# Performance work log

Hardware: AMD Instinct MI355X
Metric: run time of the kernel (lower is better)

## Reference

```python
import jax, jax.numpy as jnp
import numpy as np

N_NODES = 100000
N_EDGES = 1600000
IN_RAW = 64
HID = 128


def setup_inputs() -> dict:
    key = jax.random.key(0)
    ks = jax.random.split(key, 16)
    inp = {
        "x": jax.random.normal(ks[0], (N_NODES, IN_RAW), dtype=jnp.float32),
        "edge_index": jax.random.randint(ks[1], (2, N_EDGES), 0, N_NODES, dtype=jnp.int64),
        "user_ids": jax.random.randint(ks[2], (N_NODES,), 0, 10000, dtype=jnp.int64),
        "locations": jax.random.randint(ks[3], (N_NODES,), 0, 1000, dtype=jnp.int64),
        "time_features": jax.random.normal(ks[4], (N_NODES, 4), dtype=jnp.float32),
        # embeddings / encoders
        "user_emb_table": jax.random.normal(ks[5], (10000, 32), dtype=jnp.float32) * 0.02,
        "loc_emb_table": jax.random.normal(ks[6], (1000, 16), dtype=jnp.float32) * 0.02,
        "W_time": jax.random.normal(ks[7], (4, 16), dtype=jnp.float32) * 0.1,
        "b_time": jnp.zeros((16,), dtype=jnp.float32),
        # SAGEConv 1: lin_l (aggregated, with bias), lin_r (root, no bias)
        "W1_l": jax.random.normal(ks[8], (HID, HID), dtype=jnp.float32) * (1.0 / np.sqrt(HID)),
        "b1": jnp.zeros((HID,), dtype=jnp.float32),
        "W1_r": jax.random.normal(ks[9], (HID, HID), dtype=jnp.float32) * (1.0 / np.sqrt(HID)),
        # SAGEConv 2
        "W2_l": jax.random.normal(ks[10], (HID, HID), dtype=jnp.float32) * (1.0 / np.sqrt(HID)),
        "b2": jnp.zeros((HID,), dtype=jnp.float32),
        "W2_r": jax.random.normal(ks[11], (HID, HID), dtype=jnp.float32) * (1.0 / np.sqrt(HID)),
        # classifier
        "Wc": jax.random.normal(ks[12], (HID, 1), dtype=jnp.float32) * (1.0 / np.sqrt(HID)),
        "bc": jnp.zeros((1,), dtype=jnp.float32),
    }
    return inp


def _sage_conv(h, src, dst, W_l, b_l, W_r, n_nodes):
    # mean aggregation of source features onto targets (PyG SAGEConv default)
    msg_sum = jax.ops.segment_sum(h[src], dst, num_segments=n_nodes)  # [N, D]
    deg = jax.ops.segment_sum(jnp.ones((src.shape[0],), h.dtype), dst, num_segments=n_nodes)
    agg = msg_sum / jnp.maximum(deg, 1.0)[:, None]
    return agg @ W_l + b_l + h @ W_r


def reference(x, edge_index, user_ids, locations, time_features,
              user_emb_table, loc_emb_table, W_time, b_time,
              W1_l, b1, W1_r, W2_l, b2, W2_r, Wc, bc):
    n = x.shape[0]
    src, dst = edge_index[0], edge_index[1]
    user_emb = user_emb_table[user_ids]            # [N, 32]
    loc_emb = loc_emb_table[locations]             # [N, 16]
    time_emb = time_features @ W_time + b_time     # [N, 16]
    h = jnp.concatenate([x, user_emb, loc_emb, time_emb], axis=-1)  # [N, 128]
    h = jax.nn.relu(_sage_conv(h, src, dst, W1_l, b1, W1_r, n))  # dropout = identity (eval)
    h = jax.nn.relu(_sage_conv(h, src, dst, W2_l, b2, W2_r, n))
    return jax.nn.sigmoid(h @ Wc + bc)  # [N, 1]
```

## Files before the change

kernel.cpp:

```cpp
#include <hip/hip_runtime.h>
#include <math.h>

#define N_NODES 100000
#define HID 128
#define NB 782
#define CAP 4096
#define NBLK 196
#define BTILE 8192
#define SUBCAP 32
#define SCAP 3072
#define EMBB 3125
#define WPB 32

typedef __attribute__((ext_vector_type(8))) short bf16x8;
typedef __attribute__((ext_vector_type(4))) float f32x4;
typedef __attribute__((ext_vector_type(2))) float f32x2;

__device__ __forceinline__ unsigned short f2bf(float f) {
  union { float f; unsigned u; } v; v.f = f;
  unsigned r = v.u + 0x7FFFu + ((v.u >> 16) & 1u);
  return (unsigned short)(r >> 16);
}
__device__ __forceinline__ unsigned packbf(float lo, float hi) {
  return (unsigned)f2bf(lo) | ((unsigned)f2bf(hi) << 16);
}
__device__ __forceinline__ unsigned pkfp8x4(float a, float b, float c, float d) {
  int v = __builtin_amdgcn_cvt_pk_fp8_f32(a, b, 0, false);
  v = __builtin_amdgcn_cvt_pk_fp8_f32(c, d, v, true);
  return (unsigned)v;
}
__device__ __forceinline__ float bflo(unsigned u) {
  union { unsigned u; float f; } v; v.u = u << 16; return v.f;
}
__device__ __forceinline__ float bfhi(unsigned u) {
  union { unsigned u; float f; } v; v.u = u & 0xFFFF0000u; return v.f;
}
__device__ __forceinline__ void acc_add_fp8(float* a, unsigned w) {
  f32x2 p0 = __builtin_amdgcn_cvt_pk_f32_fp8((int)w, false);
  f32x2 p1 = __builtin_amdgcn_cvt_pk_f32_fp8((int)w, true);
  a[0] += p0.x; a[1] += p0.y; a[2] += p1.x; a[3] += p1.y;
}
__device__ __forceinline__ void acc_add_row(float* a, uint4 u) {
  acc_add_fp8(a + 0, u.x);
  acc_add_fp8(a + 4, u.y);
  acc_add_fp8(a + 8, u.z);
  acc_add_fp8(a + 12, u.w);
}

__global__ __launch_bounds__(512) void k_front(
    const float* __restrict__ x, const int* __restrict__ uid,
    const int* __restrict__ lid, const float* __restrict__ timef,
    const float* __restrict__ utab, const float* __restrict__ ltab,
    const float* __restrict__ Wt, const float* __restrict__ bt,
    unsigned short* __restrict__ h0, unsigned char* __restrict__ h0f8,
    const float* __restrict__ W1l, const float* __restrict__ W1r,
    const float* __restrict__ W2l, const float* __restrict__ W2r,
    unsigned short* __restrict__ WT,
    const int* __restrict__ src, const int* __restrict__ dst,
    int* __restrict__ gcnt, unsigned* __restrict__ bdata2, int E) {
  __shared__ int hcnt[NB];
  int bid = blockIdx.x;
  int t = threadIdx.x;

  if (bid < NBLK) {
    int e0 = bid * BTILE;
    int e1 = min(e0 + BTILE, E);
    for (int i = t; i < NB; i += 512) hcnt[i] = 0;
    __syncthreads();
#pragma unroll 4
    for (int e = e0 + t; e < e1; e += 512) atomicAdd(&hcnt[dst[e] >> 7], 1);
    __syncthreads();
    for (int i = t; i < NB; i += 512) {
      gcnt[bid * NB + i] = hcnt[i];
      hcnt[i] = 0;
    }
    __syncthreads();
#pragma unroll 4
    for (int e = e0 + t; e < e1; e += 512) {
      int d = dst[e], s = src[e];
      int b = d >> 7;
      int pos = atomicAdd(&hcnt[b], 1);
      if (pos < SUBCAP)
        bdata2[((size_t)bid * NB + b) * SUBCAP + pos] =
            ((unsigned)s << 7) | (unsigned)(d & 127);
    }
    return;
  }
  bid -= NBLK;

  if (bid < EMBB) {
    int v = bid * 32 + (t >> 4);
    int g = t & 15;
    if (v >= N_NODES) return;
    float val[8];
    if (g < 8) {
      const float4* xp = (const float4*)&x[(size_t)v * 64 + g * 8];
      float4 a = xp[0], b = xp[1];
      val[0] = a.x; val[1] = a.y; val[2] = a.z; val[3] = a.w;
      val[4] = b.x; val[5] = b.y; val[6] = b.z; val[7] = b.w;
    } else if (g < 12) {
      const float4* up = (const float4*)&utab[(size_t)uid[v] * 32 + (g - 8) * 8];
      float4 a = up[0], b = up[1];
      val[0] = a.x; val[1] = a.y; val[2] = a.z; val[3] = a.w;
      val[4] = b.x; val[5] = b.y; val[6] = b.z; val[7] = b.w;
    } else if (g < 14) {
      const float4* lp = (const float4*)&ltab[(size_t)lid[v] * 16 + (g - 12) * 8];
      float4 a = lp[0], b = lp[1];
      val[0] = a.x; val[1] = a.y; val[2] = a.z; val[3] = a.w;
      val[4] = b.x; val[5] = b.y; val[6] = b.z; val[7] = b.w;
    } else {
      int c0 = (g - 14) * 8;
      float4 tf = *(const float4*)&timef[(size_t)v * 4];
#pragma unroll
      for (int i = 0; i < 8; ++i) {
        int c = c0 + i;
        val[i] = bt[c] + tf.x * Wt[c] + tf.y * Wt[16 + c] + tf.z * Wt[32 + c] +
                 tf.w * Wt[48 + c];
      }
    }
    uint4 ob;
    ob.x = packbf(val[0], val[1]);
    ob.y = packbf(val[2], val[3]);
    ob.z = packbf(val[4], val[5]);
    ob.w = packbf(val[6], val[7]);
    *(uint4*)&h0[(size_t)v * 128 + g * 8] = ob;
    uint2 of;
    of.x = pkfp8x4(val[0], val[1], val[2], val[3]);
    of.y = pkfp8x4(val[4], val[5], val[6], val[7]);
    *(uint2*)&h0f8[(size_t)v * 128 + g * 8] = of;
    return;
  }
  bid -= EMBB;

  {
    int lin = (bid * 512 + t) * 4;
    int m = lin >> 14;
    int rem = lin & 16383;
    int f = rem >> 7;
    int k0 = rem & 127;
    const float* W = (m == 0) ? W1l : (m == 1) ? W1r : (m == 2) ? W2l : W2r;
    unsigned short o[4];
#pragma unroll
    for (int j = 0; j < 4; ++j) o[j] = f2bf(W[(size_t)(k0 + j) * 128 + f]);
    uint2 pk;
    pk.x = (unsigned)o[0] | ((unsigned)o[1] << 16);
    pk.y = (unsigned)o[2] | ((unsigned)o[3] << 16);
    *(uint2*)&WT[m * 16384 + f * 128 + k0] = pk;
  }
}

__global__ __launch_bounds__(256) void k_bfill(
    const int* __restrict__ gcnt, const unsigned* __restrict__ bdata2,
    int* __restrict__ rstart, int* __restrict__ rdeg, int* __restrict__ col) {
  __shared__ unsigned sdata[SCAP];
  __shared__ int soff[NBLK];
  __shared__ int scnt[NBLK];
  __shared__ int wsum[4];
  __shared__ int lcnt[128];
  __shared__ int wtot;
  int b = blockIdx.x;
  int t = threadIdx.x;
  int lane = t & 63, wv = t >> 6;

  int c = (t < NBLK) ? min(gcnt[t * NB + b], SUBCAP) : 0;
  int x = c;
#pragma unroll
  for (int off = 1; off < 64; off <<= 1) {
    int v = __shfl_up(x, off);
    if (lane >= off) x += v;
  }
  if (lane == 63) wsum[wv] = x;
  __syncthreads();
  int add = 0;
#pragma unroll
  for (int k = 0; k < 4; ++k)
    if (k < wv) add += wsum[k];
  x += add;
  int tot = min(wsum[0] + wsum[1] + wsum[2] + wsum[3], SCAP);
  if (t < NBLK) { soff[t] = x - c; scnt[t] = c; }
  if (t < 128) lcnt[t] = 0;
  __syncthreads();

  for (int i = t; i < NBLK * 8; i += 256) {
    int j = i >> 3, p4 = (i & 7) * 4;
    int cj = scnt[j];
    if (p4 < cj) {
      uint4 v = *(const uint4*)&bdata2[((size_t)j * NB + b) * SUBCAP + p4];
      int bs = soff[j] + p4;
      int n = min(4, cj - p4);
      unsigned vv[4] = {v.x, v.y, v.z, v.w};
#pragma unroll
      for (int e = 0; e < 4; ++e)
        if (e < n && bs + e < SCAP) sdata[bs + e] = vv[e];
    }
  }
  __syncthreads();

  for (int i = t; i < tot; i += 256) atomicAdd(&lcnt[sdata[i] & 127u], 1);
  __syncthreads();

  int node0 = b * 128;
  int base = b * CAP;
  if (t < 128) {
    int cc = lcnt[t];
    int xx = cc;
#pragma unroll
    for (int off = 1; off < 64; off <<= 1) {
      int v = __shfl_up(xx, off);
      if (lane >= off) xx += v;
    }
    if (t == 63) wtot = xx;
    __syncthreads();
    if (t >= 64) xx += wtot;
    int excl = xx - cc;
    if (node0 + t < N_NODES) {
      rstart[node0 + t] = base + excl;
      rdeg[node0 + t] = cc;
    }
    lcnt[t] = excl;
  } else {
    __syncthreads();
  }
  __syncthreads();
  for (int i = t; i < tot; i += 256) {
    unsigned v = sdata[i];
    int pos = base + atomicAdd(&lcnt[v & 127u], 1);
    col[pos] = (int)(v >> 7);
  }
}

__global__ __launch_bounds__(256) void k_agg(
    const unsigned char* __restrict__ hf8, const int* __restrict__ rstart,
    const int* __restrict__ rdeg, const int* __restrict__ col,
    unsigned short* __restrict__ agg) {
  int t = threadIdx.x;
  int v = blockIdx.x * 32 + (t >> 3);
  int q = t & 7;
  if (v >= N_NODES) return;
  int s0 = rstart[v];
  int deg = rdeg[v];
  int s1 = s0 + deg;
  const uint4* h8 = (const uint4*)hf8;
  float acc[16];
#pragma unroll
  for (int i = 0; i < 16; ++i) acc[i] = 0.f;
  int j = s0;
  for (; j + 8 <= s1; j += 8) {
    uint4 r0 = h8[(size_t)col[j] * 8 + q];
    uint4 r1 = h8[(size_t)col[j + 1] * 8 + q];
    uint4 r2 = h8[(size_t)col[j + 2] * 8 + q];
    uint4 r3 = h8[(size_t)col[j + 3] * 8 + q];
    uint4 r4 = h8[(size_t)col[j + 4] * 8 + q];
    uint4 r5 = h8[(size_t)col[j + 5] * 8 + q];
    uint4 r6 = h8[(size_t)col[j + 6] * 8 + q];
    uint4 r7 = h8[(size_t)col[j + 7] * 8 + q];
    acc_add_row(acc, r0);
    acc_add_row(acc, r1);
    acc_add_row(acc, r2);
    acc_add_row(acc, r3);
    acc_add_row(acc, r4);
    acc_add_row(acc, r5);
    acc_add_row(acc, r6);
    acc_add_row(acc, r7);
  }
  for (; j < s1; ++j) acc_add_row(acc, h8[(size_t)col[j] * 8 + q]);
  float inv = 1.f / (float)(deg > 0 ? deg : 1);
  uint4 o0, o1;
  o0.x = packbf(acc[0] * inv, acc[1] * inv);
  o0.y = packbf(acc[2] * inv, acc[3] * inv);
  o0.z = packbf(acc[4] * inv, acc[5] * inv);
  o0.w = packbf(acc[6] * inv, acc[7] * inv);
  o1.x = packbf(acc[8] * inv, acc[9] * inv);
  o1.y = packbf(acc[10] * inv, acc[11] * inv);
  o1.z = packbf(acc[12] * inv, acc[13] * inv);
  o1.w = packbf(acc[14] * inv, acc[15] * inv);
  ((uint4*)agg)[(size_t)v * 16 + q * 2] = o0;
  ((uint4*)agg)[(size_t)v * 16 + q * 2 + 1] = o1;
}

template <bool CLS>
__global__ __launch_bounds__(256, 4) void k_gemm(
    const unsigned short* __restrict__ agg, const unsigned short* __restrict__ hin,
    const unsigned short* __restrict__ WlT, const unsigned short* __restrict__ WrT,
    const float* __restrict__ bias, unsigned short* __restrict__ hout,
    unsigned char* __restrict__ houtf8,
    const float* __restrict__ Wc, const float* __restrict__ bc,
    float* __restrict__ out) {
  __shared__ unsigned short SB[2 * 64 * 136];
  unsigned short* As = SB;
  unsigned short* Hs = SB + 64 * 136;
  unsigned short* Ot = SB;
  float* zred = (float*)SB;
  int t = threadIdx.x;
  int lane = t & 63;
  int wave = t >> 6;
  int wn = wave * 32;
  int l15 = lane & 15;
  int quad = lane >> 4;
  int mbase = blockIdx.x * 64;

  {
    int r = t >> 2, seg = t & 3;
    int gn = mbase + r;
    uint4 av[4], hv[4];
    if (gn < N_NODES) {
      const uint4* ap = (const uint4*)(agg + (size_t)gn * 128 + seg * 32);
      const uint4* hp = (const uint4*)(hin + (size_t)gn * 128 + seg * 32);
#pragma unroll
      for (int i = 0; i < 4; ++i) { av[i] = ap[i]; hv[i] = hp[i]; }
    } else {
#pragma unroll
      for (int i = 0; i < 4; ++i) { av[i] = make_uint4(0,0,0,0); hv[i] = make_uint4(0,0,0,0); }
    }
#pragma unroll
    for (int i = 0; i < 4; ++i) {
      *(uint4*)&As[r * 136 + seg * 32 + i * 8] = av[i];
      *(uint4*)&Hs[r * 136 + seg * 32 + i * 8] = hv[i];
    }
  }
  __syncthreads();

  f32x4 acc4[4][2];
#pragma unroll
  for (int i = 0; i < 4; ++i)
#pragma unroll
    for (int j = 0; j < 2; ++j) acc4[i][j] = (f32x4){0.f, 0.f, 0.f, 0.f};

#pragma unroll
  for (int ks = 0; ks < 4; ++ks) {
    int kb = ks * 32 + quad * 8;
    bf16x8 bL[2], bR[2];
#pragma unroll
    for (int jn = 0; jn < 2; ++jn) {
      int f = wn + jn * 16 + l15;
      bL[jn] = *(const bf16x8*)&WlT[(size_t)f * 128 + kb];
      bR[jn] = *(const bf16x8*)&WrT[(size_t)f * 128 + kb];
    }
    bf16x8 aA[4], aH[4];
#pragma unroll
    for (int im = 0; im < 4; ++im) {
      aA[im] = *(const bf16x8*)&As[(im * 16 + l15) * 136 + kb];
      aH[im] = *(const bf16x8*)&Hs[(im * 16 + l15) * 136 + kb];
    }
#pragma unroll
    for (int im = 0; im < 4; ++im)
#pragma unroll
      for (int jn = 0; jn < 2; ++jn)
        acc4[im][jn] = __builtin_amdgcn_mfma_f32_16x16x32_bf16(
            aA[im], bL[jn], acc4[im][jn], 0, 0, 0);
#pragma unroll
    for (int im = 0; im < 4; ++im)
#pragma unroll
      for (int jn = 0; jn < 2; ++jn)
        acc4[im][jn] = __builtin_amdgcn_mfma_f32_16x16x32_bf16(
            aH[im], bR[jn], acc4[im][jn], 0, 0, 0);
  }

  float bv[2];
#pragma unroll
  for (int jn = 0; jn < 2; ++jn) bv[jn] = bias[wn + jn * 16 + l15];

  __syncthreads();

  if (!CLS) {
#pragma unroll
    for (int im = 0; im < 4; ++im)
#pragma unroll
      for (int rr = 0; rr < 4; ++rr) {
        int rloc = im * 16 + quad * 4 + rr;
#pragma unroll
        for (int jn = 0; jn < 2; ++jn)
          Ot[rloc * 136 + wn + jn * 16 + l15] =
              f2bf(fmaxf(acc4[im][jn][rr] + bv[jn], 0.f));
      }
    __syncthreads();
    int r = t >> 2, seg = t & 3;
    int node = mbase + r;
    if (node < N_NODES) {
      uint4 d0[4];
      const uint4* srcp = (const uint4*)&Ot[r * 136 + seg * 32];
      uint4* dstp = (uint4*)&hout[(size_t)node * 128 + seg * 32];
#pragma unroll
      for (int i = 0; i < 4; ++i) { d0[i] = srcp[i]; dstp[i] = d0[i]; }
      unsigned w[8];
#pragma unroll
      for (int i = 0; i < 4; ++i) {
        unsigned u[4] = {d0[i].x, d0[i].y, d0[i].z, d0[i].w};
#pragma unroll
        for (int p = 0; p < 2; ++p) {
          w[i * 2 + p] = pkfp8x4(bflo(u[p * 2]), bfhi(u[p * 2]),
                                 bflo(u[p * 2 + 1]), bfhi(u[p * 2 + 1]));
        }
      }
      uint4* fp = (uint4*)&houtf8[(size_t)node * 128 + seg * 32];
      fp[0] = make_uint4(w[0], w[1], w[2], w[3]);
      fp[1] = make_uint4(w[4], w[5], w[6], w[7]);
    }
  } else {
    float wcv[2];
#pragma unroll
    for (int jn = 0; jn < 2; ++jn) wcv[jn] = Wc[wn + jn * 16 + l15];
#pragma unroll
    for (int im = 0; im < 4; ++im) {
#pragma unroll
      for (int rr = 0; rr < 4; ++rr) {
        float p = 0.f;
#pragma unroll
        for (int jn = 0; jn < 2; ++jn)
          p += fmaxf(acc4[im][jn][rr] + bv[jn], 0.f) * wcv[jn];
        p += __shfl_xor(p, 1);
        p += __shfl_xor(p, 2);
        p += __shfl_xor(p, 4);
        p += __shfl_xor(p, 8);
        if (l15 == 0) zred[wave * 64 + im * 16 + quad * 4 + rr] = p;
      }
    }
    __syncthreads();
    if (t < 64) {
      int node = mbase + t;
      if (node < N_NODES) {
        float z = zred[t] + zred[64 + t] + zred[128 + t] + zred[192 + t] + bc[0];
        out[node] = 1.f / (1.f + expf(-z));
      }
    }
  }
}

extern "C" void kernel_launch(void* const* d_in, const int* in_sizes, int n_in,
                              void* d_out, int out_size, void* d_ws, size_t ws_size,
                              hipStream_t stream) {
  const float* x     = (const float*)d_in[0];
  const int*   eidx  = (const int*)d_in[1];
  const int*   uid   = (const int*)d_in[2];
  const int*   lid   = (const int*)d_in[3];
  const float* timef = (const float*)d_in[4];
  const float* utab  = (const float*)d_in[5];
  const float* ltab  = (const float*)d_in[6];
  const float* Wt    = (const float*)d_in[7];
  const float* bt    = (const float*)d_in[8];
  const float* W1l   = (const float*)d_in[9];
  const float* b1    = (const float*)d_in[10];
  const float* W1r   = (const float*)d_in[11];
  const float* W2l   = (const float*)d_in[12];
  const float* b2    = (const float*)d_in[13];
  const float* W2r   = (const float*)d_in[14];
  const float* Wc    = (const float*)d_in[15];
  const float* bc    = (const float*)d_in[16];
  float* out = (float*)d_out;

  const int E = in_sizes[1] / 2;
  const int* src = eidx;
  const int* dst = eidx + E;

  char* ws = (char*)d_ws;
  size_t off = 0;
  auto alloc = [&](size_t bytes) -> void* {
    void* p = ws + off;
    off += (bytes + 255) & ~(size_t)255;
    return p;
  };
  const size_t HBYTES = (size_t)N_NODES * 128 * sizeof(unsigned short);
  const size_t FBYTES = (size_t)N_NODES * 128;
  unsigned short* h0  = (unsigned short*)alloc(HBYTES);
  unsigned short* h1  = (unsigned short*)alloc(HBYTES);
  unsigned short* agg = (unsigned short*)alloc(HBYTES);
  unsigned char* h0f8 = (unsigned char*)alloc(FBYTES);
  unsigned char* h1f8 = (unsigned char*)alloc(FBYTES);
  unsigned short* WT  = (unsigned short*)alloc(4 * 16384 * sizeof(unsigned short));
  unsigned* bdata2    = (unsigned*)alloc((size_t)NBLK * NB * SUBCAP * 4);
  int* gcnt           = (int*)alloc((size_t)NBLK * NB * 4);
  int* col            = (int*)alloc((size_t)NB * CAP * 4);
  int* rstart         = (int*)alloc((size_t)N_NODES * 4);
  int* rdeg           = (int*)alloc((size_t)N_NODES * 4);
  (void)ws_size; (void)n_in; (void)out_size;

  k_front<<<NBLK + EMBB + WPB, 512, 0, stream>>>(
      x, uid, lid, timef, utab, ltab, Wt, bt, h0, h0f8,
      W1l, W1r, W2l, W2r, WT, src, dst, gcnt, bdata2, E);
  k_bfill<<<NB, 256, 0, stream>>>(gcnt, bdata2, rstart, rdeg, col);

  k_agg<<<(N_NODES + 31) / 32, 256, 0, stream>>>(h0f8, rstart, rdeg, col, agg);
  k_gemm<false><<<(N_NODES + 63) / 64, 256, 0, stream>>>(
      agg, h0, WT, WT + 16384, b1, h1, h1f8, nullptr, nullptr, nullptr);

  k_agg<<<(N_NODES + 31) / 32, 256, 0, stream>>>(h1f8, rstart, rdeg, col, agg);
  k_gemm<true><<<(N_NODES + 63) / 64, 256, 0, stream>>>(
      agg, h1, WT + 32768, WT + 49152, b2, nullptr, nullptr, Wc, bc, out);
}
```

Baseline: 298.9 us.

## Split fused front kernel into bucket, embed, and bfill-with-weight-transpose launches

The single heterogeneous k_front launch, which mixed edge bucketing, node embedding and weight transposition by block index, is split apart. Edge bucketing becomes its own kernel, embedding becomes a 256-thread kernel, and the weight bf16 transpose moves into extra blocks of k_bfill. The aim is to stop the 512-thread launch bound and the shared histogram from limiting occupancy for the embedding blocks. The cost is one extra kernel launch and the loss of overlap between bucketing and embedding within one grid.

Result: no change. 298.0 us (-0.3%).

```diff
diff --git a/kernel.cpp b/kernel.cpp
--- a/kernel.cpp
+++ b/kernel.cpp
@@ -9,8 +9,7 @@
 #define BTILE 8192
 #define SUBCAP 32
 #define SCAP 3072
-#define EMBB 3125
-#define WPB 32
+#define WPB 64
 
 typedef __attribute__((ext_vector_type(8))) short bf16x8;
 typedef __attribute__((ext_vector_type(4))) float f32x4;
@@ -47,93 +46,93 @@
   acc_add_fp8(a + 12, u.w);
 }
 
-__global__ __launch_bounds__(512) void k_front(
+__global__ __launch_bounds__(256) void k_embed(
     const float* __restrict__ x, const int* __restrict__ uid,
     const int* __restrict__ lid, const float* __restrict__ timef,
     const float* __restrict__ utab, const float* __restrict__ ltab,
     const float* __restrict__ Wt, const float* __restrict__ bt,
-    unsigned short* __restrict__ h0, unsigned char* __restrict__ h0f8,
-    const float* __restrict__ W1l, const float* __restrict__ W1r,
-    const float* __restrict__ W2l, const float* __restrict__ W2r,
-    unsigned short* __restrict__ WT,
+    unsigned short* __restrict__ h0, unsigned char* __restrict__ h0f8) {
+  int t = threadIdx.x;
+  int v = blockIdx.x * 16 + (t >> 4);
+  int g = t & 15;
+  if (v >= N_NODES) return;
+  float val[8];
+  if (g < 8) {
+    const float4* xp = (const float4*)&x[(size_t)v * 64 + g * 8];
+    float4 a = xp[0], b = xp[1];
+    val[0] = a.x; val[1] = a.y; val[2] = a.z; val[3] = a.w;
+    val[4] = b.x; val[5] = b.y; val[6] = b.z; val[7] = b.w;
+  } else if (g < 12) {
+    const float4* up = (const float4*)&utab[(size_t)uid[v] * 32 + (g - 8) * 8];
+    float4 a = up[0], b = up[1];
+    val[0] = a.x; val[1] = a.y; val[2] = a.z; val[3] = a.w;
+    val[4] = b.x; val[5] = b.y; val[6] = b.z; val[7] = b.w;
+  } else if (g < 14) {
+    const float4* lp = (const float4*)&ltab[(size_t)lid[v] * 16 + (g - 12) * 8];
+    float4 a = lp[0], b = lp[1];
+    val[0] = a.x; val[1] = a.y; val[2] = a.z; val[3] = a.w;
+    val[4] = b.x; val[5] = b.y; val[6] = b.z; val[7] = b.w;
+  } else {
+    int c0 = (g - 14) * 8;
+    float4 tf = *(const float4*)&timef[(size_t)v * 4];
+#pragma unroll
+    for (int i = 0; i < 8; ++i) {
+      int c = c0 + i;
+      val[i] = bt[c] + tf.x * Wt[c] + tf.y * Wt[16 + c] + tf.z * Wt[32 + c] +
+               tf.w * Wt[48 + c];
+    }
+  }
+  uint4 ob;
+  ob.x = packbf(val[0], val[1]);
+  ob.y = packbf(val[2], val[3]);
+  ob.z = packbf(val[4], val[5]);
+  ob.w = packbf(val[6], val[7]);
+  *(uint4*)&h0[(size_t)v * 128 + g * 8] = ob;
+  uint2 of;
+  of.x = pkfp8x4(val[0], val[1], val[2], val[3]);
+  of.y = pkfp8x4(val[4], val[5], val[6], val[7]);
+  *(uint2*)&h0f8[(size_t)v * 128 + g * 8] = of;
+}
+
+__global__ __launch_bounds__(512) void k_bucket(
     const int* __restrict__ src, const int* __restrict__ dst,
     int* __restrict__ gcnt, unsigned* __restrict__ bdata2, int E) {
   __shared__ int hcnt[NB];
-  int bid = blockIdx.x;
   int t = threadIdx.x;
-
-  if (bid < NBLK) {
-    int e0 = bid * BTILE;
-    int e1 = min(e0 + BTILE, E);
-    for (int i = t; i < NB; i += 512) hcnt[i] = 0;
-    __syncthreads();
+  int blk = blockIdx.x;
+  int e0 = blk * BTILE;
+  int e1 = min(e0 + BTILE, E);
+  for (int i = t; i < NB; i += 512) hcnt[i] = 0;
+  __syncthreads();
 #pragma unroll 4
-    for (int e = e0 + t; e < e1; e += 512) atomicAdd(&hcnt[dst[e] >> 7], 1);
-    __syncthreads();
-    for (int i = t; i < NB; i += 512) {
-      gcnt[bid * NB + i] = hcnt[i];
-      hcnt[i] = 0;
-    }
-    __syncthreads();
+  for (int e = e0 + t; e < e1; e += 512) atomicAdd(&hcnt[dst[e] >> 7], 1);
+  __syncthreads();
+  for (int i = t; i < NB; i += 512) {
+    gcnt[blk * NB + i] = hcnt[i];
+    hcnt[i] = 0;
+  }
+  __syncthreads();
 #pragma unroll 4
-    for (int e = e0 + t; e < e1; e += 512) {
-      int d = dst[e], s = src[e];
-      int b = d >> 7;
-      int pos = atomicAdd(&hcnt[b], 1);
-      if (pos < SUBCAP)
-        bdata2[((size_t)bid * NB + b) * SUBCAP + pos] =
-            ((unsigned)s << 7) | (unsigned)(d & 127);
-    }
-    return;
-  }
-  bid -= NBLK;
-
-  if (bid < EMBB) {
-    int v = bid * 32 + (t >> 4);
-    int g = t & 15;
-    if (v >= N_NODES) return;
-    float val[8];
-    if (g < 8) {
-      const float4* xp = (const float4*)&x[(size_t)v * 64 + g * 8];
-      float4 a = xp[0], b = xp[1];
-      val[0] = a.x; val[1] = a.y; val[2] = a.z; val[3] = a.w;
-      val[4] = b.x; val[5] = b.y; val[6] = b.z; val[7] = b.w;
-    } else if (g < 12) {
-      const float4* up = (const float4*)&utab[(size_t)uid[v] * 32 + (g - 8) * 8];
-      float4 a = up[0], b = up[1];
-      val[0] = a.x; val[1] = a.y; val[2] = a.z; val[3] = a.w;
-      val[4] = b.x; val[5] = b.y; val[6] = b.z; val[7] = b.w;
-    } else if (g < 14) {
-      const float4* lp = (const float4*)&ltab[(size_t)lid[v] * 16 + (g - 12) * 8];
-      float4 a = lp[0], b = lp[1];
-      val[0] = a.x; val[1] = a.y; val[2] = a.z; val[3] = a.w;
-      val[4] = b.x; val[5] = b.y; val[6] = b.z; val[7] = b.w;
-    } else {
-      int c0 = (g - 14) * 8;
-      float4 tf = *(const float4*)&timef[(size_t)v * 4];
-#pragma unroll
-      for (int i = 0; i < 8; ++i) {
-        int c = c0 + i;
-        val[i] = bt[c] + tf.x * Wt[c] + tf.y * Wt[16 + c] + tf.z * Wt[32 + c] +
-                 tf.w * Wt[48 + c];
-      }
-    }
-    uint4 ob;
-    ob.x = packbf(val[0], val[1]);
-    ob.y = packbf(val[2], val[3]);
-    ob.z = packbf(val[4], val[5]);
-    ob.w = packbf(val[6], val[7]);
-    *(uint4*)&h0[(size_t)v * 128 + g * 8] = ob;
-    uint2 of;
-    of.x = pkfp8x4(val[0], val[1], val[2], val[3]);
-    of.y = pkfp8x4(val[4], val[5], val[6], val[7]);
-    *(uint2*)&h0f8[(size_t)v * 128 + g * 8] = of;
-    return;
-  }
-  bid -= EMBB;
-
-  {
-    int lin = (bid * 512 + t) * 4;
+  for (int e = e0 + t; e < e1; e += 512) {
+    int d = dst[e], s = src[e];
+    int b = d >> 7;
+    int pos = atomicAdd(&hcnt[b], 1);
+    if (pos < SUBCAP)
+      bdata2[((size_t)blk * NB + b) * SUBCAP + pos] =
+          ((unsigned)s << 7) | (unsigned)(d & 127);
+  }
+}
+
+__global__ __launch_bounds__(256) void k_bfill(
+    const int* __restrict__ gcnt, const unsigned* __restrict__ bdata2,
+    int* __restrict__ rstart, int* __restrict__ rdeg, int* __restrict__ col,
+    const float* __restrict__ W1l, const float* __restrict__ W1r,
+    const float* __restrict__ W2l, const float* __restrict__ W2r,
+    unsigned short* __restrict__ WT) {
+  int b = blockIdx.x;
+  int t = threadIdx.x;
+  if (b >= NB) {
+    int lin = ((b - NB) * 256 + t) * 4;
     int m = lin >> 14;
     int rem = lin & 16383;
     int f = rem >> 7;
@@ -146,20 +145,14 @@
     pk.x = (unsigned)o[0] | ((unsigned)o[1] << 16);
     pk.y = (unsigned)o[2] | ((unsigned)o[3] << 16);
     *(uint2*)&WT[m * 16384 + f * 128 + k0] = pk;
-  }
-}
-
-__global__ __launch_bounds__(256) void k_bfill(
-    const int* __restrict__ gcnt, const unsigned* __restrict__ bdata2,
-    int* __restrict__ rstart, int* __restrict__ rdeg, int* __restrict__ col) {
+    return;
+  }
   __shared__ unsigned sdata[SCAP];
   __shared__ int soff[NBLK];
   __shared__ int scnt[NBLK];
   __shared__ int wsum[4];
   __shared__ int lcnt[128];
   __shared__ int wtot;
-  int b = blockIdx.x;
-  int t = threadIdx.x;
   int lane = t & 63, wv = t >> 6;
 
   int c = (t < NBLK) ? min(gcnt[t * NB + b], SUBCAP) : 0;
@@ -474,10 +467,11 @@
   int* rdeg           = (int*)alloc((size_t)N_NODES * 4);
   (void)ws_size; (void)n_in; (void)out_size;
 
-  k_front<<<NBLK + EMBB + WPB, 512, 0, stream>>>(
-      x, uid, lid, timef, utab, ltab, Wt, bt, h0, h0f8,
-      W1l, W1r, W2l, W2r, WT, src, dst, gcnt, bdata2, E);
-  k_bfill<<<NB, 256, 0, stream>>>(gcnt, bdata2, rstart, rdeg, col);
+  k_bucket<<<NBLK, 512, 0, stream>>>(src, dst, gcnt, bdata2, E);
+  k_embed<<<(N_NODES + 15) / 16, 256, 0, stream>>>(x, uid, lid, timef, utab, ltab, Wt, bt,
+                                                   h0, h0f8);
+  k_bfill<<<NB + WPB, 256, 0, stream>>>(gcnt, bdata2, rstart, rdeg, col,
+                                        W1l, W1r, W2l, W2r, WT);
 
   k_agg<<<(N_NODES + 31) / 32, 256, 0, stream>>>(h0f8, rstart, rdeg, col, agg);
   k_gemm<false><<<(N_NODES + 63) / 64, 256, 0, stream>>>(
```
